# Kernel tuning notes

Hardware: AMD Instinct MI355X
Metric: run time of the kernel (lower is better)

Reference implementation:

```python
import jax, jax.numpy as jnp
import numpy as np

N, E = 50000, 600000
IN, PE, H, L, K = 112, 16, 128, 64, 4


def setup_inputs() -> dict:
    key = jax.random.key(0)
    ks = jax.random.split(key, 8)
    x = jax.random.normal(ks[0], (N, IN), jnp.float32)
    edge_index = jax.random.randint(ks[1], (2, E), 0, N, dtype=jnp.int64)
    lap_pe = jax.random.normal(ks[2], (N, PE), jnp.float32)
    edge_weight = jax.random.uniform(ks[3], (E,), jnp.float32)
    s = lambda k, shp, fan: jax.random.normal(k, shp, jnp.float32) / np.sqrt(fan).astype(np.float32)
    W1 = s(ks[4], (K, IN + PE, H), IN + PE)
    b1 = jnp.zeros((H,), jnp.float32)
    W2 = s(ks[5], (K, H, H), H)
    b2 = jnp.zeros((H,), jnp.float32)
    Wmu = s(ks[6], (H, L), H)
    bmu = jnp.zeros((L,), jnp.float32)
    Wlv = s(ks[7], (H, L), H)
    blv = jnp.zeros((L,), jnp.float32)
    return dict(x=x, edge_index=edge_index, lap_pe=lap_pe, edge_weight=edge_weight,
                W1=W1, b1=b1, W2=W2, b2=b2, Wmu=Wmu, bmu=bmu, Wlv=Wlv, blv=blv)


def _cheb_conv(h, src, dst, w, W, b):
    """PyG ChebConv with precomputed scaled-Laplacian edge weights w.
    T_0 = h ; T_1 = That h ; T_k = 2 That T_{k-1} - T_{k-2}; out = sum_k T_k W_k + b."""
    n = h.shape[0]
    prop = lambda t: jax.ops.segment_sum(w[:, None] * t[src], dst, num_segments=n)
    Tx0 = h
    out = Tx0 @ W[0]
    Tx1 = prop(Tx0)
    out = out + Tx1 @ W[1]
    for k in range(2, W.shape[0]):
        Tx2 = 2.0 * prop(Tx1) - Tx0
        out = out + Tx2 @ W[k]
        Tx0, Tx1 = Tx1, Tx2
    return out + b


def reference(x, edge_index, lap_pe, edge_weight, W1, b1, W2, b2, Wmu, bmu, Wlv, blv):
    n = x.shape[0]
    src, dst = edge_index[0], edge_index[1]
    # sym-normalized Laplacian, lambda_max=2 -> That = L_sym - I = -D^-1/2 A D^-1/2
    deg = jax.ops.segment_sum(edge_weight, src, num_segments=n)
    dis = jnp.where(deg > 0, jax.lax.rsqrt(jnp.maximum(deg, 1e-12)), 0.0)
    w = -dis[src] * edge_weight * dis[dst]
    h = jnp.concatenate([x, lap_pe], axis=1)  # [N, in+pe]
    h = jax.nn.relu(_cheb_conv(h, src, dst, w, W1, b1))
    h = jax.nn.relu(_cheb_conv(h, src, dst, w, W2, b2))
    mu = h @ Wmu + bmu
    logvar = h @ Wlv + blv
    return (mu, logvar)
```

## Files before the change

kernel.cpp:

```cpp
#include <hip/hip_runtime.h>


typedef __bf16 bf16x8 __attribute__((ext_vector_type(8)));
typedef float f32x4 __attribute__((ext_vector_type(4)));
typedef unsigned int uint32;
typedef unsigned short ushort16;

__device__ inline ushort16 f2bf(float f) {
    uint32 x = __float_as_uint(f);
    uint32 r = x + 0x7fffu + ((x >> 16) & 1u);
    return (ushort16)(r >> 16);
}
__device__ inline float bflo(uint32 v) { return __uint_as_float(v << 16); }
__device__ inline float bfhi(uint32 v) { return __uint_as_float(v & 0xffff0000u); }


__global__ void k_deg_cnt(const int* __restrict__ src, const int* __restrict__ dst,
                          const float* __restrict__ ew, float* __restrict__ deg,
                          int* __restrict__ cnt, int* __restrict__ pos,
                          int e0, int e1) {
    int e = e0 + blockIdx.x * blockDim.x + threadIdx.x;
    if (e >= e1) return;
    atomicAdd(&deg[src[e]], ew[e]);
    pos[e] = atomicAdd(&cnt[dst[e]], 1);
}

__global__ void k_scan_blk(const int* __restrict__ cnt, int* __restrict__ row_ptr,
                           int* __restrict__ blk_sums, int N) {
    __shared__ int wsum[4];
    const int tid = threadIdx.x;
    const int base = blockIdx.x * 1024 + tid * 4;
    int4 v = make_int4(0, 0, 0, 0);
    if (base + 3 < N) v = *(const int4*)&cnt[base];
    else {
        if (base + 0 < N) v.x = cnt[base + 0];
        if (base + 1 < N) v.y = cnt[base + 1];
        if (base + 2 < N) v.z = cnt[base + 2];
    }
    const int tsum = v.x + v.y + v.z + v.w;
    const int lane = tid & 63;
    const int wv = tid >> 6;
    int incl = tsum;
    #pragma unroll
    for (int off = 1; off < 64; off <<= 1) {
        int t = __shfl_up(incl, off);
        if (lane >= off) incl += t;
    }
    if (lane == 63) wsum[wv] = incl;
    __syncthreads();
    int woff = 0;
    #pragma unroll
    for (int w = 0; w < 4; ++w) if (w < wv) woff += wsum[w];
    const int excl = woff + incl - tsum;
    if (base + 0 < N) row_ptr[base + 0] = excl;
    if (base + 1 < N) row_ptr[base + 1] = excl + v.x;
    if (base + 2 < N) row_ptr[base + 2] = excl + v.x + v.y;
    if (base + 3 < N) row_ptr[base + 3] = excl + v.x + v.y + v.z;
    if (tid == 255) blk_sums[blockIdx.x] = woff + incl;
}

__global__ void k_scan_top(int* __restrict__ blk_sums, int* __restrict__ row_ptr,
                           int nblk, int N) {
    const int lane = threadIdx.x;
    int v = (lane < nblk) ? blk_sums[lane] : 0;
    int incl = v;
    #pragma unroll
    for (int off = 1; off < 64; off <<= 1) {
        int t = __shfl_up(incl, off);
        if (lane >= off) incl += t;
    }
    if (lane < nblk) blk_sums[lane] = incl - v;
    if (lane == 63) row_ptr[N] = incl;
}

__global__ void k_fix_dis(int* __restrict__ row_ptr, const int* __restrict__ blk_sums,
                          const float* __restrict__ deg, float* __restrict__ dis, int N) {
    int i = blockIdx.x * blockDim.x + threadIdx.x;
    if (i >= N) return;
    row_ptr[i] += blk_sums[i >> 10];
    float d = deg[i];
    dis[i] = d > 0.f ? rsqrtf(fmaxf(d, 1e-12f)) : 0.f;
}

__global__ void k_scatter(const int* __restrict__ src, const int* __restrict__ dst,
                          const float* __restrict__ ew, const float* __restrict__ dis,
                          const int* __restrict__ row_ptr, const int* __restrict__ pos,
                          int2* __restrict__ csr, int E) {
    int e = blockIdx.x * blockDim.x + threadIdx.x;
    if (e >= E) return;
    int s = src[e], d = dst[e];
    float wv = -dis[s] * ew[e] * dis[d];
    csr[row_ptr[d] + pos[e]] = make_int2(s, __float_as_int(wv));
}


__global__ void k_concat_bf16(const float* __restrict__ x, const float* __restrict__ pe,
                              uint32* __restrict__ h, int N) {
    int i4 = (blockIdx.x * blockDim.x + threadIdx.x) * 4;
    if (i4 >= N * 64) return;
    int node = i4 >> 6, p = i4 & 63;
    float4 fa, fb;
    if (p < 56) {
        const float* xp = &x[(size_t)node * 112 + p * 2];
        fa = *(const float4*)xp; fb = *(const float4*)(xp + 4);
    } else {
        const float* pp = &pe[(size_t)node * 16 + (p - 56) * 2];
        fa = *(const float4*)pp; fb = *(const float4*)(pp + 4);
    }
    int4 o;
    o.x = (uint32)f2bf(fa.x) | ((uint32)f2bf(fa.y) << 16);
    o.y = (uint32)f2bf(fa.z) | ((uint32)f2bf(fa.w) << 16);
    o.z = (uint32)f2bf(fb.x) | ((uint32)f2bf(fb.y) << 16);
    o.w = (uint32)f2bf(fb.z) | ((uint32)f2bf(fb.w) << 16);
    *(int4*)&h[i4] = o;
}


__device__ inline float wtrans(const float* __restrict__ W, int kb, size_t o) {
    switch (kb) {
        case 0:  return W[o] - W[o + 32768];
        case 1:  return W[o + 16384] - 3.f * W[o + 49152];
        case 2:  return 2.f * W[o + 32768];
        default: return 4.f * W[o + 49152];
    }
}

__global__ void k_pack_all(const float* __restrict__ W1, const float* __restrict__ W2,
                           const float* __restrict__ Wm, const float* __restrict__ Wl,
                           ushort16* __restrict__ W1p, ushort16* __restrict__ W2p,
                           ushort16* __restrict__ WHp) {
    int t = blockIdx.x * blockDim.x + threadIdx.x;
    uint32 v[8];
    if (t < 16384) {
        const float* W = (t < 8192) ? W1 : W2;
        ushort16* Wp = (t < 8192) ? W1p : W2p;
        int tt = t & 8191;
        int l = tt & 63, c = (tt >> 6) & 7, ks = tt >> 9;
        int kb = ks >> 2;
        int r0 = (ks & 3) * 32 + (l >> 4) * 8;
        int col = c * 16 + (l & 15);
        #pragma unroll
        for (int j = 0; j < 8; ++j)
            v[j] = f2bf(wtrans(W, kb, (size_t)(r0 + j) * 128 + col));
        uint4 o;
        o.x = v[0] | (v[1] << 16); o.y = v[2] | (v[3] << 16);
        o.z = v[4] | (v[5] << 16); o.w = v[6] | (v[7] << 16);
        *(uint4*)(Wp + (size_t)tt * 8) = o;
    } else if (t < 16384 + 2048) {
        int tt = t - 16384;
        int l = tt & 63, c = (tt >> 6) & 7, ks = tt >> 9;
        int k0 = ks * 32 + (l >> 4) * 8;
        int cc = c * 16 + (l & 15);
        const float* Ws = (cc < 64) ? Wm : Wl;
        int col = cc & 63;
        #pragma unroll
        for (int j = 0; j < 8; ++j) v[j] = f2bf(Ws[(size_t)(k0 + j) * 64 + col]);
        uint4 o;
        o.x = v[0] | (v[1] << 16); o.y = v[2] | (v[3] << 16);
        o.z = v[4] | (v[5] << 16); o.w = v[6] | (v[7] << 16);
        *(uint4*)(WHp + (size_t)tt * 8) = o;
    }
}


__global__ void k_prop(const uint32* __restrict__ tin, const int2* __restrict__ csr,
                       const int* __restrict__ row_ptr, uint32* __restrict__ out, int N) {
    int wave = (blockIdx.x * blockDim.x + threadIdx.x) >> 6;
    int lane = threadIdx.x & 63;
    const int half = lane >> 5;
    const int fl = lane & 31;
    int node = wave * 2 + half;
    bool valid = node < N;
    if (!valid) node = N - 1;
    int beg = row_ptr[node];
    int m = valid ? (row_ptr[node + 1] - beg) : 0;
    float a0 = 0.f, a1 = 0.f, a2 = 0.f, a3 = 0.f;
    for (int base = 0; base < m; base += 32) {
        int rem = m - base; if (rem > 32) rem = 32;
        int2 ev = (fl < rem) ? csr[beg + base + fl] : make_int2(0, 0);
        for (int j = 0; j < rem; j += 8) {
            #pragma unroll
            for (int u = 0; u < 8; ++u) {
                int s = __shfl(ev.x, half * 32 + j + u);
                float w = __uint_as_float(__shfl(ev.y, half * 32 + j + u));
                uint2 v = *(const uint2*)&tin[(size_t)s * 64 + fl * 2];
                a0 = fmaf(w, bflo(v.x), a0); a1 = fmaf(w, bfhi(v.x), a1);
                a2 = fmaf(w, bflo(v.y), a2); a3 = fmaf(w, bfhi(v.y), a3);
            }
        }
    }
    if (valid) {
        uint2 o;
        o.x = (uint32)f2bf(a0) | ((uint32)f2bf(a1) << 16);
        o.y = (uint32)f2bf(a2) | ((uint32)f2bf(a3) << 16);
        *(uint2*)&out[(size_t)node * 64 + fl * 2] = o;
    }
}


template<bool RELU>
__launch_bounds__(256)
__global__ void k_mfma_gemm512(const ushort16* __restrict__ t0, const ushort16* __restrict__ t1,
                               const ushort16* __restrict__ t2, const ushort16* __restrict__ t3,
                               const ushort16* __restrict__ Wp, const float* __restrict__ bias,
                               ushort16* __restrict__ C, int N) {
    const int lane = threadIdx.x & 63;
    const int wave = threadIdx.x >> 6;
    const int brow = blockIdx.x * 128 + wave * 32;
    int r0 = brow + (lane & 15);
    int r1 = r0 + 16;
    if (r0 >= N) r0 = N - 1;
    if (r1 >= N) r1 = N - 1;
    const int kg8 = (lane >> 4) * 8;
    f32x4 acc[2][8] = {};
    #pragma unroll
    for (int t = 0; t < 4; ++t) {
        const ushort16* __restrict__ A = (t == 0) ? t0 : (t == 1) ? t1 : (t == 2) ? t2 : t3;
        const ushort16* a0p = A + (size_t)r0 * 128 + kg8;
        const ushort16* a1p = A + (size_t)r1 * 128 + kg8;
        #pragma unroll
        for (int ks2 = 0; ks2 < 4; ++ks2) {
            bf16x8 a0 = *(const bf16x8*)(a0p + ks2 * 32);
            bf16x8 a1 = *(const bf16x8*)(a1p + ks2 * 32);
            const ushort16* bp = Wp + (size_t)((t * 4 + ks2) * 8 * 64 + lane) * 8;
            #pragma unroll
            for (int c = 0; c < 8; ++c) {
                bf16x8 b = *(const bf16x8*)(bp + c * 512);
                acc[0][c] = __builtin_amdgcn_mfma_f32_16x16x32_bf16(a0, b, acc[0][c], 0, 0, 0);
                acc[1][c] = __builtin_amdgcn_mfma_f32_16x16x32_bf16(a1, b, acc[1][c], 0, 0, 0);
            }
        }
    }
    const int col0 = lane & 15;
    const int rj = (lane >> 4) * 4;
    #pragma unroll
    for (int m = 0; m < 2; ++m) {
        #pragma unroll
        for (int c = 0; c < 8; ++c) {
            float bv = bias[c * 16 + col0];
            #pragma unroll
            for (int j = 0; j < 4; ++j) {
                int row = brow + m * 16 + rj + j;
                if (row < N) {
                    float v = acc[m][c][j] + bv;
                    if (RELU) v = fmaxf(v, 0.f);
                    C[(size_t)row * 128 + c * 16 + col0] = f2bf(v);
                }
            }
        }
    }
}


__launch_bounds__(256)
__global__ void k_mfma_head(const ushort16* __restrict__ A, const ushort16* __restrict__ Wp,
                            const float* __restrict__ bm, const float* __restrict__ bl,
                            float* __restrict__ out, int N) {
    const int lane = threadIdx.x & 63;
    const int wave = threadIdx.x >> 6;
    const int brow = blockIdx.x * 128 + wave * 32;
    int r0 = brow + (lane & 15);
    int r1 = r0 + 16;
    if (r0 >= N) r0 = N - 1;
    if (r1 >= N) r1 = N - 1;
    const int kg8 = (lane >> 4) * 8;
    f32x4 acc[2][8] = {};
    const ushort16* a0p = A + (size_t)r0 * 128 + kg8;
    const ushort16* a1p = A + (size_t)r1 * 128 + kg8;
    #pragma unroll
    for (int ks = 0; ks < 4; ++ks) {
        bf16x8 a0 = *(const bf16x8*)(a0p + ks * 32);
        bf16x8 a1 = *(const bf16x8*)(a1p + ks * 32);
        const ushort16* bp = Wp + (size_t)(ks * 8 * 64 + lane) * 8;
        #pragma unroll
        for (int c = 0; c < 8; ++c) {
            bf16x8 b = *(const bf16x8*)(bp + c * 512);
            acc[0][c] = __builtin_amdgcn_mfma_f32_16x16x32_bf16(a0, b, acc[0][c], 0, 0, 0);
            acc[1][c] = __builtin_amdgcn_mfma_f32_16x16x32_bf16(a1, b, acc[1][c], 0, 0, 0);
        }
    }
    const int col0 = lane & 15;
    const int rj = (lane >> 4) * 4;
    #pragma unroll
    for (int m = 0; m < 2; ++m) {
        #pragma unroll
        for (int c = 0; c < 8; ++c) {
            int gcol = (c & 3) * 16 + col0;
            float bv = (c < 4) ? bm[gcol] : bl[gcol];
            size_t hoff = (c < 4) ? 0 : (size_t)N * 64;
            #pragma unroll
            for (int j = 0; j < 4; ++j) {
                int row = brow + m * 16 + rj + j;
                if (row < N)
                    out[hoff + (size_t)row * 64 + gcol] = acc[m][c][j] + bv;
            }
        }
    }
}


extern "C" void kernel_launch(void* const* d_in, const int* in_sizes, int n_in,
                              void* d_out, int out_size, void* d_ws, size_t ws_size,
                              hipStream_t stream) {
    const float* x   = (const float*)d_in[0];
    const int*   ei  = (const int*)d_in[1];
    const float* pe  = (const float*)d_in[2];
    const float* ew  = (const float*)d_in[3];
    const float* W1  = (const float*)d_in[4];
    const float* b1  = (const float*)d_in[5];
    const float* W2  = (const float*)d_in[6];
    const float* b2  = (const float*)d_in[7];
    const float* Wmu = (const float*)d_in[8];
    const float* bmu = (const float*)d_in[9];
    const float* Wlv = (const float*)d_in[10];
    const float* blv = (const float*)d_in[11];

    const int N = in_sizes[0] / 112;
    const int E = in_sizes[1] / 2;
    const int* src = ei;
    const int* dst = ei + E;

    char* ws = (char*)d_ws;
    size_t off = 0;
    auto alloc = [&](size_t bytes) -> char* {
        char* p = ws + off;
        off = (off + bytes + 255) & ~(size_t)255;
        return p;
    };
    float* deg     = (float*)alloc((size_t)N * 4);
    int*   cnt     = (int*)  alloc((size_t)N * 4);
    float* dis     = (float*)alloc((size_t)N * 4);
    int*   row_ptr = (int*)  alloc((size_t)(N + 1) * 4);
    int*   blk_sums= (int*)  alloc((size_t)256 * 4);
    int*   pos     = (int*)  alloc((size_t)E * 4);
    int2*  csr     = (int2*) alloc((size_t)E * 8);
    ushort16* W1p  = (ushort16*)alloc((size_t)512 * 128 * 2);
    ushort16* W2p  = (ushort16*)alloc((size_t)512 * 128 * 2);
    ushort16* WHp  = (ushort16*)alloc((size_t)128 * 128 * 2);
    ushort16* B0 = (ushort16*)alloc((size_t)N * 128 * 2);
    ushort16* B1 = (ushort16*)alloc((size_t)N * 128 * 2);
    ushort16* B2 = (ushort16*)alloc((size_t)N * 128 * 2);
    ushort16* B3 = (ushort16*)alloc((size_t)N * 128 * 2);
    ushort16* B4 = (ushort16*)alloc((size_t)N * 128 * 2);

    hipMemsetAsync(deg, 0, (size_t)N * 4, stream);
    hipMemsetAsync(cnt, 0, (size_t)N * 4, stream);

    const int eb4 = (E / 4 + 255) / 256;
    const int nb = (N + 255) / 256;
    const int pb = ((N + 1) / 2 + 3) / 4;
    const int gb = (N + 127) / 128;
    const int nblk = (N + 1023) / 1024;
    const int cb = (N * 64 + 1023) / 1024;

    for (int q = 0; q < 4; ++q) {
        int e0 = (int)((size_t)E * q / 4);
        int e1 = (int)((size_t)E * (q + 1) / 4);
        k_deg_cnt<<<eb4, 256, 0, stream>>>(src, dst, ew, deg, cnt, pos, e0, e1);
    }
    k_scan_blk<<<nblk, 256, 0, stream>>>(cnt, row_ptr, blk_sums, N);
    k_scan_top<<<1, 64, 0, stream>>>(blk_sums, row_ptr, nblk, N);
    k_fix_dis<<<nb, 256, 0, stream>>>(row_ptr, blk_sums, deg, dis, N);
    k_scatter<<<(E + 255) / 256, 256, 0, stream>>>(src, dst, ew, dis, row_ptr, pos, csr, E);
    k_concat_bf16<<<cb, 256, 0, stream>>>(x, pe, (uint32*)B0, N);
    k_pack_all<<<(16384 + 2048 + 255) / 256, 256, 0, stream>>>(W1, W2, Wmu, Wlv, W1p, W2p, WHp);

    k_prop<<<pb, 256, 0, stream>>>((uint32*)B0, csr, row_ptr, (uint32*)B1, N);
    k_prop<<<pb, 256, 0, stream>>>((uint32*)B1, csr, row_ptr, (uint32*)B2, N);
    k_prop<<<pb, 256, 0, stream>>>((uint32*)B2, csr, row_ptr, (uint32*)B3, N);
    k_mfma_gemm512<true><<<gb, 256, 0, stream>>>(B0, B1, B2, B3, W1p, b1, B4, N);

    k_prop<<<pb, 256, 0, stream>>>((uint32*)B4, csr, row_ptr, (uint32*)B0, N);
    k_prop<<<pb, 256, 0, stream>>>((uint32*)B0, csr, row_ptr, (uint32*)B1, N);
    k_prop<<<pb, 256, 0, stream>>>((uint32*)B1, csr, row_ptr, (uint32*)B2, N);
    k_mfma_gemm512<true><<<gb, 256, 0, stream>>>(B4, B0, B1, B2, W2p, b2, B3, N);

    k_mfma_head<<<gb, 256, 0, stream>>>(B3, WHp, bmu, blv, (float*)d_out, N);
}
```

Before: 312.0 us.

## Use one wave per node in SpMM and stage GEMM A tiles in LDS

The propagation kernel now assigns a full 64-lane wave to each node. Each lane gathers one packed bf16 pair per neighbor instead of two half-waves sharing a node with 8-byte loads, and the grid is resized to match. The fused Chebyshev GEMM now loads each 128-row A tile into shared memory with coalesced 16-byte loads and an XOR swizzle, then reads MFMA fragments from LDS rather than issuing strided global loads per lane. This adds block-wide barriers per T_k term and halves the number of nodes per wave in the gather.

```diff
diff --git a/kernel.cpp b/kernel.cpp
--- a/kernel.cpp
+++ b/kernel.cpp
@@ -165,36 +165,25 @@
 
 __global__ void k_prop(const uint32* __restrict__ tin, const int2* __restrict__ csr,
                        const int* __restrict__ row_ptr, uint32* __restrict__ out, int N) {
-    int wave = (blockIdx.x * blockDim.x + threadIdx.x) >> 6;
+    int wid = (blockIdx.x * blockDim.x + threadIdx.x) >> 6;
     int lane = threadIdx.x & 63;
-    const int half = lane >> 5;
-    const int fl = lane & 31;
-    int node = wave * 2 + half;
-    bool valid = node < N;
-    if (!valid) node = N - 1;
-    int beg = row_ptr[node];
-    int m = valid ? (row_ptr[node + 1] - beg) : 0;
-    float a0 = 0.f, a1 = 0.f, a2 = 0.f, a3 = 0.f;
-    for (int base = 0; base < m; base += 32) {
-        int rem = m - base; if (rem > 32) rem = 32;
-        int2 ev = (fl < rem) ? csr[beg + base + fl] : make_int2(0, 0);
-        for (int j = 0; j < rem; j += 8) {
+    if (wid >= N) return;
+    int beg = row_ptr[wid], end = row_ptr[wid + 1];
+    float ax = 0.f, ay = 0.f;
+    for (int base = beg; base < end; base += 64) {
+        int m = end - base; if (m > 64) m = 64;
+        int2 ev = (lane < m) ? csr[base + lane] : make_int2(0, 0);
+        for (int j = 0; j < m; j += 8) {
             #pragma unroll
             for (int u = 0; u < 8; ++u) {
-                int s = __shfl(ev.x, half * 32 + j + u);
-                float w = __uint_as_float(__shfl(ev.y, half * 32 + j + u));
-                uint2 v = *(const uint2*)&tin[(size_t)s * 64 + fl * 2];
-                a0 = fmaf(w, bflo(v.x), a0); a1 = fmaf(w, bfhi(v.x), a1);
-                a2 = fmaf(w, bflo(v.y), a2); a3 = fmaf(w, bfhi(v.y), a3);
+                int s = __shfl(ev.x, j + u);
+                float w = __uint_as_float(__shfl(ev.y, j + u));
+                uint32 v = tin[(size_t)s * 64 + lane];
+                ax = fmaf(w, bflo(v), ax); ay = fmaf(w, bfhi(v), ay);
             }
         }
     }
-    if (valid) {
-        uint2 o;
-        o.x = (uint32)f2bf(a0) | ((uint32)f2bf(a1) << 16);
-        o.y = (uint32)f2bf(a2) | ((uint32)f2bf(a3) << 16);
-        *(uint2*)&out[(size_t)node * 64 + fl * 2] = o;
-    }
+    out[(size_t)wid * 64 + lane] = (uint32)f2bf(ax) | ((uint32)f2bf(ay) << 16);
 }
 
 
@@ -204,24 +193,36 @@
                                const ushort16* __restrict__ t2, const ushort16* __restrict__ t3,
                                const ushort16* __restrict__ Wp, const float* __restrict__ bias,
                                ushort16* __restrict__ C, int N) {
+    __shared__ char lds_a[32768];
     const int lane = threadIdx.x & 63;
     const int wave = threadIdx.x >> 6;
-    const int brow = blockIdx.x * 128 + wave * 32;
-    int r0 = brow + (lane & 15);
-    int r1 = r0 + 16;
-    if (r0 >= N) r0 = N - 1;
-    if (r1 >= N) r1 = N - 1;
+    const int brow = blockIdx.x * 128;
+    const int orow = brow + wave * 32;
+    const int fr0 = wave * 32 + (lane & 15);
+    const int fr1 = fr0 + 16;
     const int kg8 = (lane >> 4) * 8;
+    const int sl0 = lane >> 4;
     f32x4 acc[2][8] = {};
-    #pragma unroll
+    const ushort16* As[4] = {t0, t1, t2, t3};
+
     for (int t = 0; t < 4; ++t) {
-        const ushort16* __restrict__ A = (t == 0) ? t0 : (t == 1) ? t1 : (t == 2) ? t2 : t3;
-        const ushort16* a0p = A + (size_t)r0 * 128 + kg8;
-        const ushort16* a1p = A + (size_t)r1 * 128 + kg8;
+        const ushort16* __restrict__ A = As[t];
+        __syncthreads();
+        #pragma unroll
+        for (int i = 0; i < 8; ++i) {
+            int q = wave * 8 + i;
+            int r = q * 4 + (lane >> 4);
+            int gr = brow + r; if (gr >= N) gr = N - 1;
+            int slot = (lane & 15) ^ (r & 7);
+            uint4 v = *(const uint4*)((const char*)(A + (size_t)gr * 128) + slot * 16);
+            *(uint4*)(lds_a + r * 256 + (lane & 15) * 16) = v;
+        }
+        __syncthreads();
         #pragma unroll
         for (int ks2 = 0; ks2 < 4; ++ks2) {
-            bf16x8 a0 = *(const bf16x8*)(a0p + ks2 * 32);
-            bf16x8 a1 = *(const bf16x8*)(a1p + ks2 * 32);
+            int ls = ks2 * 4 + sl0;
+            bf16x8 a0 = *(const bf16x8*)(lds_a + fr0 * 256 + ((ls ^ (fr0 & 7)) * 16));
+            bf16x8 a1 = *(const bf16x8*)(lds_a + fr1 * 256 + ((ls ^ (fr1 & 7)) * 16));
             const ushort16* bp = Wp + (size_t)((t * 4 + ks2) * 8 * 64 + lane) * 8;
             #pragma unroll
             for (int c = 0; c < 8; ++c) {
@@ -240,7 +241,7 @@
             float bv = bias[c * 16 + col0];
             #pragma unroll
             for (int j = 0; j < 4; ++j) {
-                int row = brow + m * 16 + rj + j;
+                int row = orow + m * 16 + rj + j;
                 if (row < N) {
                     float v = acc[m][c][j] + bv;
                     if (RELU) v = fmaxf(v, 0.f);
@@ -348,7 +349,7 @@
 
     const int eb4 = (E / 4 + 255) / 256;
     const int nb = (N + 255) / 256;
-    const int pb = ((N + 1) / 2 + 3) / 4;
+    const int pb = (N + 3) / 4;
     const int gb = (N + 127) / 128;
     const int nblk = (N + 1023) / 1024;
     const int cb = (N * 64 + 1023) / 1024;
```

Result: slower. 334.9 us (+7.3%).
